# Kernel tuning notes

Hardware: AMD Instinct MI355X
Metric: run time of the kernel (lower is better)

Reference implementation:

```python
import jax, jax.numpy as jnp
import numpy as np
import math

B, S, E, H = 2, 2048, 1024, 16
D = E // H  # head_dim = 64
WINDOW = 512
EPS = 1e-5


def _layernorm(x, gamma, beta):
    mu = jnp.mean(x, axis=-1, keepdims=True)
    var = jnp.var(x, axis=-1, keepdims=True)
    return (x - mu) * jax.lax.rsqrt(var + EPS) * gamma + beta


def setup_inputs() -> dict:
    key = jax.random.key(0)
    ks = jax.random.split(key, 5)
    return {
        "x": jax.random.normal(ks[0], (B, S, E), jnp.float32),
        "W_qkv": jax.random.normal(ks[1], (E, 3 * E), jnp.float32) * (E ** -0.5),
        "b_qkv": jax.random.normal(ks[2], (3 * E,), jnp.float32) * 0.02,
        "q_gamma": jnp.ones((D,), jnp.float32),
        "q_beta": jnp.zeros((D,), jnp.float32),
        "k_gamma": jnp.ones((D,), jnp.float32),
        "k_beta": jnp.zeros((D,), jnp.float32),
        "W_out": jax.random.normal(ks[3], (E, E), jnp.float32) * (E ** -0.5),
        "b_out": jax.random.normal(ks[4], (E,), jnp.float32) * 0.02,
    }


def reference(x, W_qkv, b_qkv, q_gamma, q_beta, k_gamma, k_beta, W_out, b_out):
    b, s, e = x.shape
    # fused QKV projection -> (3, B, H, S, D)
    qkv = (x @ W_qkv + b_qkv).reshape(b, s, 3, H, D).transpose(2, 0, 3, 1, 4)
    q, k, v = qkv[0], qkv[1], qkv[2]
    # qk_norm: LayerNorm over head_dim
    q = _layernorm(q, q_gamma, q_beta)
    k = _layernorm(k, k_gamma, k_beta)
    scores = jnp.einsum("bhqd,bhkd->bhqk", q, k) / math.sqrt(D)
    # causal + sliding-window mask (True = masked out)
    row = jnp.arange(s)[:, None]
    col = jnp.arange(s)[None, :]
    masked = (col > row) | (row - col >= WINDOW)  # sliding window subsumes causal
    scores = jnp.where(masked[None, None], -jnp.inf, scores)
    attn = jax.nn.softmax(scores, axis=-1)
    out = jnp.einsum("bhqk,bhkd->bhqd", attn, v)  # (B,H,S,D)
    out = out.transpose(0, 2, 1, 3).reshape(b, s, e)
    return out @ W_out + b_out
```

## Files before the change

### kernel.cpp

```cpp
#include <hip/hip_runtime.h>
#include <stdint.h>

typedef uint16_t u16;
typedef __attribute__((ext_vector_type(8))) short short8;
typedef __attribute__((ext_vector_type(4))) float f32x4;

#define DEV static __device__ __forceinline__

DEV u16 f2bf(float f) {
  uint32_t u = __float_as_uint(f);
  return (u16)((u + 0x7fffu + ((u >> 16) & 1u)) >> 16);
}
DEV float bf2f(u16 h) { return __uint_as_float(((uint32_t)h) << 16); }

DEV void gload16(const void* g, void* l) {
  __builtin_amdgcn_global_load_lds(
      (const __attribute__((address_space(1))) void*)g,
      (__attribute__((address_space(3))) void*)l, 16, 0, 0);
}

__global__ void k_cast4(const float* __restrict__ in, u16* __restrict__ out, int n4) {
  int i = blockIdx.x * blockDim.x + threadIdx.x;
  if (i >= n4) return;
  float4 v = ((const float4*)in)[i];
  uint2 p;
  p.x = (uint32_t)f2bf(v.x) | ((uint32_t)f2bf(v.y) << 16);
  p.y = (uint32_t)f2bf(v.z) | ((uint32_t)f2bf(v.w) << 16);
  ((uint2*)out)[i] = p;
}

__global__ void k_tcast(const float* __restrict__ Wm, u16* __restrict__ Wt, int K, int N) {
  __shared__ u16 t[64][65];
  int n0 = blockIdx.x * 64, k0 = blockIdx.y * 64;
  int tid = threadIdx.x;
#pragma unroll
  for (int i = 0; i < 16; ++i) {
    int idx = tid + i * 256, r = idx >> 6, c = idx & 63;
    t[r][c] = f2bf(Wm[(size_t)(k0 + r) * N + n0 + c]);
  }
  __syncthreads();
#pragma unroll
  for (int i = 0; i < 16; ++i) {
    int idx = tid + i * 256, r = idx >> 6, c = idx & 63;
    Wt[(size_t)(n0 + r) * K + k0 + c] = t[c][r];
  }
}

__global__ __launch_bounds__(256) void k_gemmqkv(
    const u16* __restrict__ A, const u16* __restrict__ Bt,
    const float* __restrict__ bias,
    const float* __restrict__ qg, const float* __restrict__ qb,
    const float* __restrict__ kg, const float* __restrict__ kb,
    u16* __restrict__ Qn, u16* __restrict__ Kn, u16* __restrict__ Vt) {
  const int K = 1024, N = 3072;
  __shared__ __attribute__((aligned(16))) u16 S[2][2][128 * 64];
  int bid = blockIdx.x;
  int ntn = N >> 7;
  int cpx = gridDim.x >> 3;
  int wg = (bid & 7) * cpx + (bid >> 3);
  int my = wg / ntn, nx = wg - my * ntn;
  int m0 = my * 128, n0 = nx * 128;
  int tid = threadIdx.x, lane = tid & 63, w = tid >> 6;
  int wr = (w >> 1) * 64, wc = (w & 1) * 64;
  int lr = lane & 15, lg = lane >> 4;
  int rsw = (lr & 7) << 3;
  int srow = tid >> 3;
  int scb = ((tid & 7) ^ ((tid >> 3) & 7)) * 8;
  f32x4 acc[4][4];
#pragma unroll
  for (int i = 0; i < 4; ++i)
#pragma unroll
    for (int j = 0; j < 4; ++j) acc[i][j] = (f32x4){0.f, 0.f, 0.f, 0.f};

  int nk = K >> 6;

#define STGQ(buf, kt)                                                                   \
  do {                                                                                  \
    gload16(A + (size_t)(m0 + srow) * K + (kt) * 64 + scb, &S[buf][0][tid * 8]);        \
    gload16(A + (size_t)(m0 + 32 + srow) * K + (kt) * 64 + scb, &S[buf][0][2048 + tid * 8]);  \
    gload16(A + (size_t)(m0 + 64 + srow) * K + (kt) * 64 + scb, &S[buf][0][4096 + tid * 8]);  \
    gload16(A + (size_t)(m0 + 96 + srow) * K + (kt) * 64 + scb, &S[buf][0][6144 + tid * 8]);  \
    gload16(Bt + (size_t)(n0 + srow) * K + (kt) * 64 + scb, &S[buf][1][tid * 8]);       \
    gload16(Bt + (size_t)(n0 + 32 + srow) * K + (kt) * 64 + scb, &S[buf][1][2048 + tid * 8]); \
    gload16(Bt + (size_t)(n0 + 64 + srow) * K + (kt) * 64 + scb, &S[buf][1][4096 + tid * 8]); \
    gload16(Bt + (size_t)(n0 + 96 + srow) * K + (kt) * 64 + scb, &S[buf][1][6144 + tid * 8]); \
  } while (0)

  STGQ(0, 0);
  asm volatile("s_waitcnt vmcnt(0)" ::: "memory");
  __syncthreads();

  for (int t = 0; t < nk; ++t) {
    int cur = t & 1;
    if (t + 1 < nk) STGQ(cur ^ 1, t + 1);
#pragma unroll
    for (int ks = 0; ks < 2; ++ks) {
      short8 af[4], bf[4];
#pragma unroll
      for (int mi = 0; mi < 4; ++mi)
        af[mi] = *(const short8*)&S[cur][0][((wr + mi * 16 + lr) * 64 + ks * 32 + lg * 8) ^ rsw];
#pragma unroll
      for (int ni = 0; ni < 4; ++ni)
        bf[ni] = *(const short8*)&S[cur][1][((wc + ni * 16 + lr) * 64 + ks * 32 + lg * 8) ^ rsw];
      __builtin_amdgcn_s_setprio(1);
#pragma unroll
      for (int mi = 0; mi < 4; ++mi)
#pragma unroll
        for (int ni = 0; ni < 4; ++ni)
          acc[mi][ni] = __builtin_amdgcn_mfma_f32_16x16x32_bf16(af[mi], bf[ni], acc[mi][ni], 0, 0, 0);
      __builtin_amdgcn_s_setprio(0);
    }
    asm volatile("s_waitcnt vmcnt(0)" ::: "memory");
    __syncthreads();
  }
#undef STGQ

  int rg = lg * 4;
  int sec = n0 >> 10;
  int hh = ((n0 + wc) >> 6) & 15;
  int b = m0 >> 11;
  int s0 = m0 & 2047;

  if (sec < 2) {
    const float* gp = sec ? kg : qg;
    const float* bp = sec ? kb : qb;
    float scl = sec ? 1.f : (0.125f * 1.44269504f);
    u16* op = sec ? Kn : Qn;
    float gv[4], bev[4], bb[4];
#pragma unroll
    for (int ni = 0; ni < 4; ++ni) {
      int d = ni * 16 + lr;
      gv[ni] = gp[d];
      bev[ni] = bp[d];
      bb[ni] = bias[n0 + wc + d];
    }
    size_t hb = (size_t)(b * 16 + hh) * 2048 * 64;
#pragma unroll
    for (int mi = 0; mi < 4; ++mi) {
      float a[4][4], ps[4], ps2[4];
#pragma unroll
      for (int ni = 0; ni < 4; ++ni)
#pragma unroll
        for (int j = 0; j < 4; ++j) a[ni][j] = acc[mi][ni][j] + bb[ni];
#pragma unroll
      for (int j = 0; j < 4; ++j) {
        ps[j] = a[0][j] + a[1][j] + a[2][j] + a[3][j];
        ps2[j] = a[0][j] * a[0][j] + a[1][j] * a[1][j] + a[2][j] * a[2][j] + a[3][j] * a[3][j];
      }
#pragma unroll
      for (int m = 1; m < 16; m <<= 1)
#pragma unroll
        for (int j = 0; j < 4; ++j) {
          ps[j] += __shfl_xor(ps[j], m, 64);
          ps2[j] += __shfl_xor(ps2[j], m, 64);
        }
#pragma unroll
      for (int j = 0; j < 4; ++j) {
        float mean = ps[j] * (1.f / 64);
        float var = ps2[j] * (1.f / 64) - mean * mean;
        float r = rsqrtf(var + 1e-5f);
        int row = s0 + wr + mi * 16 + rg + j;
        size_t base = hb + (size_t)row * 64;
#pragma unroll
        for (int ni = 0; ni < 4; ++ni) {
          float v = ((a[ni][j] - mean) * r * gv[ni] + bev[ni]) * scl;
          op[base + ni * 16 + lr] = f2bf(v);
        }
      }
    }
  } else {
    u16* vbase = Vt + (size_t)(b * 16 + hh) * 64 * 2048;
#pragma unroll
    for (int ni = 0; ni < 4; ++ni) {
      int d = ni * 16 + lr;
      float bb = bias[n0 + wc + d];
#pragma unroll
      for (int mi = 0; mi < 4; ++mi) {
        int row0 = s0 + wr + mi * 16 + rg;
        uint2 pk;
        pk.x = (uint32_t)f2bf(acc[mi][ni][0] + bb) | ((uint32_t)f2bf(acc[mi][ni][1] + bb) << 16);
        pk.y = (uint32_t)f2bf(acc[mi][ni][2] + bb) | ((uint32_t)f2bf(acc[mi][ni][3] + bb) << 16);
        *(uint2*)(vbase + (size_t)d * 2048 + row0) = pk;
      }
    }
  }
}

template <int OUT_BF16>
__global__ __launch_bounds__(256) void k_gemm4(
    const u16* __restrict__ A, const u16* __restrict__ Bt,
    const float* __restrict__ bias, void* __restrict__ Cout,
    int M, int N, int K) {
  __shared__ __attribute__((aligned(16))) u16 S[2][2][128 * 64];
  int bid = blockIdx.x;
  int ntn = N >> 7;
  int cpx = gridDim.x >> 3;
  int wg = (bid & 7) * cpx + (bid >> 3);
  int my = wg / ntn, nx = wg - my * ntn;
  int m0 = my * 128, n0 = nx * 128;
  int tid = threadIdx.x, lane = tid & 63, w = tid >> 6;
  int wr = (w >> 1) * 64, wc = (w & 1) * 64;
  int lr = lane & 15, lg = lane >> 4;
  int rsw = (lr & 7) << 3;
  int srow = tid >> 3;
  int scb = ((tid & 7) ^ ((tid >> 3) & 7)) * 8;
  f32x4 acc[4][4];
#pragma unroll
  for (int i = 0; i < 4; ++i)
#pragma unroll
    for (int j = 0; j < 4; ++j) acc[i][j] = (f32x4){0.f, 0.f, 0.f, 0.f};

  int nk = K >> 6;

#define STG4(buf, kt)                                                                   \
  do {                                                                                  \
    gload16(A + (size_t)(m0 + srow) * K + (kt) * 64 + scb, &S[buf][0][tid * 8]);        \
    gload16(A + (size_t)(m0 + 32 + srow) * K + (kt) * 64 + scb, &S[buf][0][2048 + tid * 8]);  \
    gload16(A + (size_t)(m0 + 64 + srow) * K + (kt) * 64 + scb, &S[buf][0][4096 + tid * 8]);  \
    gload16(A + (size_t)(m0 + 96 + srow) * K + (kt) * 64 + scb, &S[buf][0][6144 + tid * 8]);  \
    gload16(Bt + (size_t)(n0 + srow) * K + (kt) * 64 + scb, &S[buf][1][tid * 8]);       \
    gload16(Bt + (size_t)(n0 + 32 + srow) * K + (kt) * 64 + scb, &S[buf][1][2048 + tid * 8]); \
    gload16(Bt + (size_t)(n0 + 64 + srow) * K + (kt) * 64 + scb, &S[buf][1][4096 + tid * 8]); \
    gload16(Bt + (size_t)(n0 + 96 + srow) * K + (kt) * 64 + scb, &S[buf][1][6144 + tid * 8]); \
  } while (0)

  STG4(0, 0);
  asm volatile("s_waitcnt vmcnt(0)" ::: "memory");
  __syncthreads();

  for (int t = 0; t < nk; ++t) {
    int cur = t & 1;
    if (t + 1 < nk) STG4(cur ^ 1, t + 1);
#pragma unroll
    for (int ks = 0; ks < 2; ++ks) {
      short8 af[4], bf[4];
#pragma unroll
      for (int mi = 0; mi < 4; ++mi)
        af[mi] = *(const short8*)&S[cur][0][((wr + mi * 16 + lr) * 64 + ks * 32 + lg * 8) ^ rsw];
#pragma unroll
      for (int ni = 0; ni < 4; ++ni)
        bf[ni] = *(const short8*)&S[cur][1][((wc + ni * 16 + lr) * 64 + ks * 32 + lg * 8) ^ rsw];
      __builtin_amdgcn_s_setprio(1);
#pragma unroll
      for (int mi = 0; mi < 4; ++mi)
#pragma unroll
        for (int ni = 0; ni < 4; ++ni)
          acc[mi][ni] = __builtin_amdgcn_mfma_f32_16x16x32_bf16(af[mi], bf[ni], acc[mi][ni], 0, 0, 0);
      __builtin_amdgcn_s_setprio(0);
    }
    asm volatile("s_waitcnt vmcnt(0)" ::: "memory");
    __syncthreads();
  }
#undef STG4

  int rg = lg * 4;
#pragma unroll
  for (int mi = 0; mi < 4; ++mi) {
#pragma unroll
    for (int ni = 0; ni < 4; ++ni) {
      int col = n0 + wc + ni * 16 + lr;
      float bv = bias[col];
#pragma unroll
      for (int j = 0; j < 4; ++j) {
        int row = m0 + wr + mi * 16 + rg + j;
        float o = acc[mi][ni][j] + bv;
        if (OUT_BF16) ((u16*)Cout)[(size_t)row * N + col] = f2bf(o);
        else ((float*)Cout)[(size_t)row * N + col] = o;
      }
    }
  }
}

__global__ __launch_bounds__(256) void k_attn7(
    const u16* __restrict__ Qn, const u16* __restrict__ Kn,
    const u16* __restrict__ Vt, u16* __restrict__ attb) {
  __shared__ __attribute__((aligned(16))) u16 KL[2][4096];
  __shared__ __attribute__((aligned(16))) u16 VL[2][4096];
  __shared__ __attribute__((aligned(16))) u16 Pl[4][2304];
  int bid = blockIdx.x;
  int xcd = bid & 7, idx = bid >> 3;
  int bh = xcd * 4 + (idx & 3);
  int qb = 15 - (idx >> 2);
  int q0 = qb * 128;
  int tid = threadIdx.x, lane = tid & 63, w = tid >> 6;
  int ln15 = lane & 15, lg = lane >> 4;
  int qlo = q0 + w * 32;
  const u16* Qh = Qn + (size_t)bh * (2048 * 64);
  const u16* Kh = Kn + (size_t)bh * (2048 * 64);
  const u16* Vh = Vt + (size_t)bh * (64 * 2048);
  int rsw = (ln15 & 7) << 3;
  int srow = tid >> 3;
  int scb = ((tid & 7) ^ ((tid >> 3) & 7)) * 8;

  short8 qf[2][2];
#pragma unroll
  for (int qs = 0; qs < 2; ++qs)
#pragma unroll
    for (int h2 = 0; h2 < 2; ++h2)
      qf[qs][h2] = *(const short8*)(Qh + (size_t)(qlo + qs * 16 + ln15) * 64 + h2 * 32 + lg * 8);

  f32x4 oacc[2][4];
#pragma unroll
  for (int qs = 0; qs < 2; ++qs)
#pragma unroll
    for (int dt = 0; dt < 4; ++dt) oacc[qs][dt] = (f32x4){0.f, 0.f, 0.f, 0.f};
  float lwp[2][4];
#pragma unroll
  for (int qs = 0; qs < 2; ++qs)
#pragma unroll
    for (int j = 0; j < 4; ++j) lwp[qs][j] = 0.f;

  int t0 = q0 >= 512 ? (q0 - 511) >> 6 : 0;
  int t1 = (q0 + 127) >> 6;

#define STAGE_A7(buf, kt)                                                              \
  do {                                                                                 \
    const u16* Kt_ = Kh + (size_t)(kt) * 4096;                                         \
    gload16(Kt_ + (size_t)srow * 64 + scb, &KL[buf][tid * 8]);                         \
    gload16(Kt_ + (size_t)(srow + 32) * 64 + scb, &KL[buf][2048 + tid * 8]);           \
    const u16* Vt_ = Vh + (size_t)(kt) * 64;                                           \
    gload16(Vt_ + (size_t)srow * 2048 + scb, &VL[buf][tid * 8]);                       \
    gload16(Vt_ + (size_t)(srow + 32) * 2048 + scb, &VL[buf][2048 + tid * 8]);         \
  } while (0)

  STAGE_A7(0, t0);
  asm volatile("s_waitcnt vmcnt(0)" ::: "memory");
  __syncthreads();

  for (int t = t0; t <= t1; ++t) {
    int cur = (t - t0) & 1;
    if (t + 1 <= t1) STAGE_A7(cur ^ 1, t + 1);
    int kt6 = t * 64;
    if (kt6 <= qlo + 31 && kt6 + 63 >= qlo - 511) {
      short8 kf[4][2];
#pragma unroll
      for (int c = 0; c < 4; ++c)
#pragma unroll
        for (int h2 = 0; h2 < 2; ++h2)
          kf[c][h2] = *(const short8*)&KL[cur][((c * 16 + ln15) * 64 + h2 * 32 + lg * 8) ^ rsw];
      f32x4 sf[2][4];
      __builtin_amdgcn_s_setprio(1);
#pragma unroll
      for (int qs = 0; qs < 2; ++qs)
#pragma unroll
        for (int c = 0; c < 4; ++c) {
          f32x4 z = (f32x4){0.f, 0.f, 0.f, 0.f};
          z = __builtin_amdgcn_mfma_f32_16x16x32_bf16(qf[qs][0], kf[c][0], z, 0, 0, 0);
          sf[qs][c] = __builtin_amdgcn_mfma_f32_16x16x32_bf16(qf[qs][1], kf[c][1], z, 0, 0, 0);
        }
      __builtin_amdgcn_s_setprio(0);
      bool interior = (kt6 + 63 <= qlo) && (kt6 >= qlo - 480);
      if (interior) {
#pragma unroll
        for (int qs = 0; qs < 2; ++qs)
#pragma unroll
          for (int c = 0; c < 4; ++c)
#pragma unroll
            for (int j = 0; j < 4; ++j) {
              float p = __builtin_amdgcn_exp2f(sf[qs][c][j]);
              sf[qs][c][j] = p;
              lwp[qs][j] += p;
            }
      } else {
#pragma unroll
        for (int qs = 0; qs < 2; ++qs)
#pragma unroll
          for (int c = 0; c < 4; ++c) {
            int kk = kt6 + c * 16 + ln15;
#pragma unroll
            for (int j = 0; j < 4; ++j) {
              int q = qlo + qs * 16 + lg * 4 + j;
              bool msk = (kk > q) || ((q - kk) >= 512);
              float p = __builtin_amdgcn_exp2f(msk ? -1e30f : sf[qs][c][j]);
              sf[qs][c][j] = p;
              lwp[qs][j] += p;
            }
          }
      }
#pragma unroll
      for (int qs = 0; qs < 2; ++qs)
#pragma unroll
        for (int c = 0; c < 4; ++c)
#pragma unroll
          for (int j = 0; j < 4; ++j) {
            uint32_t u = __float_as_uint(sf[qs][c][j]);
            Pl[w][(qs * 16 + lg * 4 + j) * 72 + c * 16 + ln15] = (u16)((u + 0x8000u) >> 16);
          }
      short8 vf[4][2];
#pragma unroll
      for (int dt = 0; dt < 4; ++dt)
#pragma unroll
        for (int h2 = 0; h2 < 2; ++h2)
          vf[dt][h2] = *(const short8*)&VL[cur][((dt * 16 + ln15) * 64 + h2 * 32 + lg * 8) ^ rsw];
      __builtin_amdgcn_s_setprio(1);
#pragma unroll
      for (int qs = 0; qs < 2; ++qs)
#pragma unroll
        for (int h2 = 0; h2 < 2; ++h2) {
          short8 pf = *(const short8*)&Pl[w][(qs * 16 + ln15) * 72 + h2 * 32 + lg * 8];
#pragma unroll
          for (int dt = 0; dt < 4; ++dt)
            oacc[qs][dt] = __builtin_amdgcn_mfma_f32_16x16x32_bf16(pf, vf[dt][h2], oacc[qs][dt], 0, 0, 0);
        }
      __builtin_amdgcn_s_setprio(0);
    }
    asm volatile("s_waitcnt vmcnt(0)" ::: "memory");
    __syncthreads();
  }
#undef STAGE_A7

  int b = bh >> 4, hh = bh & 15;
#pragma unroll
  for (int qs = 0; qs < 2; ++qs)
#pragma unroll
    for (int j = 0; j < 4; ++j) {
      float rs = lwp[qs][j];
#pragma unroll
      for (int m = 8; m > 0; m >>= 1) rs += __shfl_xor(rs, m, 64);
      float inv = rs > 0.f ? 1.f / rs : 0.f;
      int row = b * 2048 + qlo + qs * 16 + lg * 4 + j;
#pragma unroll
      for (int dt = 0; dt < 4; ++dt)
        attb[(size_t)row * 1024 + hh * 64 + dt * 16 + ln15] = f2bf(oacc[qs][dt][j] * inv);
    }
}

extern "C" void kernel_launch(void* const* d_in, const int* in_sizes, int n_in,
                              void* d_out, int out_size, void* d_ws, size_t ws_size,
                              hipStream_t stream) {
  const float* x = (const float*)d_in[0];
  const float* Wqkv = (const float*)d_in[1];
  const float* bqkv = (const float*)d_in[2];
  const float* qg = (const float*)d_in[3];
  const float* qb = (const float*)d_in[4];
  const float* kg = (const float*)d_in[5];
  const float* kb = (const float*)d_in[6];
  const float* Wout = (const float*)d_in[7];
  const float* bout = (const float*)d_in[8];
  float* out = (float*)d_out;

  char* ws = (char*)d_ws;
  u16* attb = (u16*)(ws);
  u16* Vt = (u16*)(ws + 8388608);
  u16* Qn = (u16*)(ws + 16777216);
  u16* Kn = (u16*)(ws + 25165824);
  u16* xb = (u16*)(ws + 33554432);
  u16* wqkvT = (u16*)(ws + 41943040);
  u16* woutT = (u16*)(ws + 48234496);

  k_cast4<<<4096, 256, 0, stream>>>(x, xb, 4194304 / 4);
  k_tcast<<<dim3(48, 16), 256, 0, stream>>>(Wqkv, wqkvT, 1024, 3072);
  k_tcast<<<dim3(16, 16), 256, 0, stream>>>(Wout, woutT, 1024, 1024);
  k_gemmqkv<<<768, 256, 0, stream>>>(xb, wqkvT, bqkv, qg, qb, kg, kb, Qn, Kn, Vt);
  k_attn7<<<512, 256, 0, stream>>>(Qn, Kn, Vt, attb);
  k_gemm4<0><<<256, 256, 0, stream>>>(attb, woutT, bout, out, 4096, 1024, 1024);
}
```

Before: 99.74 us.

## Enlarge QKV GEMM tile to 256x256 with 8 waves and deeper prefetch

The QKV projection GEMM moves from 128x128 tiles with 4 waves to 256x256 tiles with 8 waves per block (grid 768 to 192), and each wave now computes 128x64. The load pipeline changes to issue two stages ahead, waiting with vmcnt(8) instead of draining after every k-step. The aim is more operand reuse per LDS byte and better hiding of global-load latency. In exchange it uses 128KB of LDS and more accumulator registers, and 192 blocks may underfill the 256 CUs.

```diff
diff --git a/kernel.cpp b/kernel.cpp
--- a/kernel.cpp
+++ b/kernel.cpp
@@ -46,76 +46,85 @@
   }
 }
 
-__global__ __launch_bounds__(256) void k_gemmqkv(
+__global__ __launch_bounds__(512) void k_gemmqkv8(
     const u16* __restrict__ A, const u16* __restrict__ Bt,
     const float* __restrict__ bias,
     const float* __restrict__ qg, const float* __restrict__ qb,
     const float* __restrict__ kg, const float* __restrict__ kb,
     u16* __restrict__ Qn, u16* __restrict__ Kn, u16* __restrict__ Vt) {
   const int K = 1024, N = 3072;
-  __shared__ __attribute__((aligned(16))) u16 S[2][2][128 * 64];
+  __shared__ __attribute__((aligned(16))) u16 SA[2][16384];
+  __shared__ __attribute__((aligned(16))) u16 SB[2][16384];
   int bid = blockIdx.x;
-  int ntn = N >> 7;
+  int ntn = N >> 8;
   int cpx = gridDim.x >> 3;
   int wg = (bid & 7) * cpx + (bid >> 3);
   int my = wg / ntn, nx = wg - my * ntn;
-  int m0 = my * 128, n0 = nx * 128;
+  int m0 = my * 256, n0 = nx * 256;
   int tid = threadIdx.x, lane = tid & 63, w = tid >> 6;
-  int wr = (w >> 1) * 64, wc = (w & 1) * 64;
+  int wm = w >> 2, wn = w & 3;
+  int wr = wm * 128, wc = wn * 64;
   int lr = lane & 15, lg = lane >> 4;
   int rsw = (lr & 7) << 3;
   int srow = tid >> 3;
   int scb = ((tid & 7) ^ ((tid >> 3) & 7)) * 8;
-  f32x4 acc[4][4];
-#pragma unroll
-  for (int i = 0; i < 4; ++i)
+  f32x4 acc[8][4];
+#pragma unroll
+  for (int i = 0; i < 8; ++i)
 #pragma unroll
     for (int j = 0; j < 4; ++j) acc[i][j] = (f32x4){0.f, 0.f, 0.f, 0.f};
 
   int nk = K >> 6;
 
-#define STGQ(buf, kt)                                                                   \
-  do {                                                                                  \
-    gload16(A + (size_t)(m0 + srow) * K + (kt) * 64 + scb, &S[buf][0][tid * 8]);        \
-    gload16(A + (size_t)(m0 + 32 + srow) * K + (kt) * 64 + scb, &S[buf][0][2048 + tid * 8]);  \
-    gload16(A + (size_t)(m0 + 64 + srow) * K + (kt) * 64 + scb, &S[buf][0][4096 + tid * 8]);  \
-    gload16(A + (size_t)(m0 + 96 + srow) * K + (kt) * 64 + scb, &S[buf][0][6144 + tid * 8]);  \
-    gload16(Bt + (size_t)(n0 + srow) * K + (kt) * 64 + scb, &S[buf][1][tid * 8]);       \
-    gload16(Bt + (size_t)(n0 + 32 + srow) * K + (kt) * 64 + scb, &S[buf][1][2048 + tid * 8]); \
-    gload16(Bt + (size_t)(n0 + 64 + srow) * K + (kt) * 64 + scb, &S[buf][1][4096 + tid * 8]); \
-    gload16(Bt + (size_t)(n0 + 96 + srow) * K + (kt) * 64 + scb, &S[buf][1][6144 + tid * 8]); \
+#define STG8(buf, kt)                                                                    \
+  do {                                                                                   \
+    gload16(A + (size_t)(m0 + srow) * K + (kt) * 64 + scb, &SA[buf][tid * 8]);           \
+    gload16(A + (size_t)(m0 + 64 + srow) * K + (kt) * 64 + scb, &SA[buf][4096 + tid * 8]);   \
+    gload16(A + (size_t)(m0 + 128 + srow) * K + (kt) * 64 + scb, &SA[buf][8192 + tid * 8]);  \
+    gload16(A + (size_t)(m0 + 192 + srow) * K + (kt) * 64 + scb, &SA[buf][12288 + tid * 8]); \
+    gload16(Bt + (size_t)(n0 + srow) * K + (kt) * 64 + scb, &SB[buf][tid * 8]);          \
+    gload16(Bt + (size_t)(n0 + 64 + srow) * K + (kt) * 64 + scb, &SB[buf][4096 + tid * 8]);  \
+    gload16(Bt + (size_t)(n0 + 128 + srow) * K + (kt) * 64 + scb, &SB[buf][8192 + tid * 8]); \
+    gload16(Bt + (size_t)(n0 + 192 + srow) * K + (kt) * 64 + scb, &SB[buf][12288 + tid * 8]); \
   } while (0)
 
-  STGQ(0, 0);
-  asm volatile("s_waitcnt vmcnt(0)" ::: "memory");
-  __syncthreads();
+  STG8(0, 0);
+  STG8(1, 1);
 
   for (int t = 0; t < nk; ++t) {
     int cur = t & 1;
-    if (t + 1 < nk) STGQ(cur ^ 1, t + 1);
+    if (t + 1 < nk)
+      asm volatile("s_waitcnt vmcnt(8)" ::: "memory");
+    else
+      asm volatile("s_waitcnt vmcnt(0)" ::: "memory");
+    __syncthreads();
 #pragma unroll
     for (int ks = 0; ks < 2; ++ks) {
-      short8 af[4], bf[4];
-#pragma unroll
-      for (int mi = 0; mi < 4; ++mi)
-        af[mi] = *(const short8*)&S[cur][0][((wr + mi * 16 + lr) * 64 + ks * 32 + lg * 8) ^ rsw];
+      short8 bfr[4];
 #pragma unroll
       for (int ni = 0; ni < 4; ++ni)
-        bf[ni] = *(const short8*)&S[cur][1][((wc + ni * 16 + lr) * 64 + ks * 32 + lg * 8) ^ rsw];
-      __builtin_amdgcn_s_setprio(1);
-#pragma unroll
-      for (int mi = 0; mi < 4; ++mi)
-#pragma unroll
-        for (int ni = 0; ni < 4; ++ni)
-          acc[mi][ni] = __builtin_amdgcn_mfma_f32_16x16x32_bf16(af[mi], bf[ni], acc[mi][ni], 0, 0, 0);
-      __builtin_amdgcn_s_setprio(0);
-    }
-    asm volatile("s_waitcnt vmcnt(0)" ::: "memory");
+        bfr[ni] = *(const short8*)&SB[cur][((wc + ni * 16 + lr) * 64 + ks * 32 + lg * 8) ^ rsw];
+#pragma unroll
+      for (int mh = 0; mh < 2; ++mh) {
+        short8 afr[4];
+#pragma unroll
+        for (int a = 0; a < 4; ++a)
+          afr[a] = *(const short8*)&SA[cur][((wr + (mh * 4 + a) * 16 + lr) * 64 + ks * 32 + lg * 8) ^ rsw];
+        __builtin_amdgcn_s_setprio(1);
+#pragma unroll
+        for (int a = 0; a < 4; ++a)
+#pragma unroll
+          for (int ni = 0; ni < 4; ++ni)
+            acc[mh * 4 + a][ni] =
+                __builtin_amdgcn_mfma_f32_16x16x32_bf16(afr[a], bfr[ni], acc[mh * 4 + a][ni], 0, 0, 0);
+        __builtin_amdgcn_s_setprio(0);
+      }
+    }
     __syncthreads();
-  }
-#undef STGQ
-
-  int rg = lg * 4;
+    if (t + 2 < nk) STG8(cur, t + 2);
+  }
+#undef STG8
+
   int sec = n0 >> 10;
   int hh = ((n0 + wc) >> 6) & 15;
   int b = m0 >> 11;
@@ -136,7 +145,7 @@
     }
     size_t hb = (size_t)(b * 16 + hh) * 2048 * 64;
 #pragma unroll
-    for (int mi = 0; mi < 4; ++mi) {
+    for (int mi = 0; mi < 8; ++mi) {
       float a[4][4], ps[4], ps2[4];
 #pragma unroll
       for (int ni = 0; ni < 4; ++ni)
@@ -159,7 +168,7 @@
         float mean = ps[j] * (1.f / 64);
         float var = ps2[j] * (1.f / 64) - mean * mean;
         float r = rsqrtf(var + 1e-5f);
-        int row = s0 + wr + mi * 16 + rg + j;
+        int row = s0 + wr + mi * 16 + lg * 4 + j;
         size_t base = hb + (size_t)row * 64;
 #pragma unroll
         for (int ni = 0; ni < 4; ++ni) {
@@ -175,8 +184,8 @@
       int d = ni * 16 + lr;
       float bb = bias[n0 + wc + d];
 #pragma unroll
-      for (int mi = 0; mi < 4; ++mi) {
-        int row0 = s0 + wr + mi * 16 + rg;
+      for (int mi = 0; mi < 8; ++mi) {
+        int row0 = s0 + wr + mi * 16 + lg * 4;
         uint2 pk;
         pk.x = (uint32_t)f2bf(acc[mi][ni][0] + bb) | ((uint32_t)f2bf(acc[mi][ni][1] + bb) << 16);
         pk.y = (uint32_t)f2bf(acc[mi][ni][2] + bb) | ((uint32_t)f2bf(acc[mi][ni][3] + bb) << 16);
@@ -451,7 +460,7 @@
   k_cast4<<<4096, 256, 0, stream>>>(x, xb, 4194304 / 4);
   k_tcast<<<dim3(48, 16), 256, 0, stream>>>(Wqkv, wqkvT, 1024, 3072);
   k_tcast<<<dim3(16, 16), 256, 0, stream>>>(Wout, woutT, 1024, 1024);
-  k_gemmqkv<<<768, 256, 0, stream>>>(xb, wqkvT, bqkv, qg, qb, kg, kb, Qn, Kn, Vt);
+  k_gemmqkv8<<<192, 512, 0, stream>>>(xb, wqkvT, bqkv, qg, qb, kg, kb, Qn, Kn, Vt);
   k_attn7<<<512, 256, 0, stream>>>(Qn, Kn, Vt, attb);
   k_gemm4<0><<<256, 256, 0, stream>>>(attb, woutT, bout, out, 4096, 1024, 1024);
 }
```

Result: no change. 100.7 us (+0.9%).
